# Performance work log

Hardware: AMD Instinct MI355X
Metric: run time of the kernel (lower is better)

The kernel has to match this reference:

```python
import jax, jax.numpy as jnp
import numpy as np
from jax import lax

B, N, NCAM, NLVL = 2, 65536, 5, 3
CIN, MID, OUT, PTSC = 256, 128, 128, 128
H, W = 64, 112
EPS = 1e-3


def setup_inputs() -> dict:
    ks = jax.random.split(jax.random.key(0), 8)
    f32 = jnp.float32
    img_feats = jax.random.normal(ks[0], (NLVL, B * NCAM, CIN, H, W), f32)
    # points roughly in front of the cameras (z ~ 15) so many project in-bounds
    pts_xyz = jax.random.normal(ks[1], (B, N, 3), f32) * 10.0 + jnp.array([0.0, 0.0, 15.0], f32)
    cam_ids = jnp.sort(jax.random.randint(ks[2], (B, N), 0, NCAM), axis=1).astype(jnp.int32)
    pts_feats = jax.random.normal(ks[3], (B * N, PTSC), f32)
    T = jnp.broadcast_to(jnp.eye(4, dtype=f32), (NCAM, 4, 4))
    T = T.at[:, :3, 3].set(jax.random.normal(ks[4], (NCAM, 3), f32) * 0.5)
    fx, fy, cx, cy = 400.0, 400.0, 4.0 * W, 4.0 * H  # full-res intrinsics (feature stride 8)
    K = jnp.broadcast_to(jnp.array([[fx, 0.0, cx], [0.0, fy, cy], [0.0, 0.0, 1.0]], f32), (NCAM, 3, 3))
    conv_w = jax.random.normal(ks[5], (NLVL, MID, CIN, 3, 3), f32) * 0.02
    conv_b = jnp.zeros((NLVL, MID), f32)
    img_w = jax.random.normal(ks[6], (OUT, MID * NLVL), f32) * 0.05
    img_b = jnp.zeros((OUT,), f32)
    img_gamma = jnp.ones((OUT,), f32)
    img_beta = jnp.zeros((OUT,), f32)
    pts_w = jax.random.normal(ks[7], (OUT, PTSC), f32) * 0.05
    pts_b = jnp.zeros((OUT,), f32)
    pts_gamma = jnp.ones((OUT,), f32)
    pts_beta = jnp.zeros((OUT,), f32)
    return dict(img_feats=img_feats, pts_xyz=pts_xyz, pts_feats=pts_feats, T=T, K=K,
                conv_w=conv_w, conv_b=conv_b, img_w=img_w, img_b=img_b,
                img_gamma=img_gamma, img_beta=img_beta, pts_w=pts_w, pts_b=pts_b,
                pts_gamma=pts_gamma, pts_beta=pts_beta, cam_ids=cam_ids)


def _bn(x, gamma, beta):
    # BatchNorm1d in training mode: batch statistics, biased variance, eps=1e-3
    mu = jnp.mean(x, axis=0)
    var = jnp.var(x, axis=0)
    return (x - mu) * lax.rsqrt(var + EPS) * gamma + beta


def _bilinear(feat, bidx, cam, px, py):
    # feat: [B, NCAM, H, W, C]; px/py: [B, N] pixel coords (align_corners=True)
    # grid_sample bilinear with zeros padding: out-of-bounds corners contribute 0
    x0f = jnp.floor(px)
    y0f = jnp.floor(py)
    wx1 = px - x0f
    wy1 = py - y0f

    def corner(xf, yf, wgt):
        valid = (xf >= 0) & (xf <= W - 1) & (yf >= 0) & (yf <= H - 1)
        xi = jnp.clip(xf, 0, W - 1).astype(jnp.int32)
        yi = jnp.clip(yf, 0, H - 1).astype(jnp.int32)
        v = feat[bidx, cam, yi, xi]  # [B, N, C]
        return v * (wgt * valid)[..., None]

    return (corner(x0f, y0f, (1 - wx1) * (1 - wy1))
            + corner(x0f + 1, y0f, wx1 * (1 - wy1))
            + corner(x0f, y0f + 1, (1 - wx1) * wy1)
            + corner(x0f + 1, y0f + 1, wx1 * wy1))


def _forward(img_feats, pts_xyz, pts_feats, T, K, conv_w, conv_b, img_w, img_b,
             img_gamma, img_beta, pts_w, pts_b, pts_gamma, pts_beta, cam_ids):
    # scale intrinsics to the 1/8-resolution feature maps (K[0,0],K[0,2],K[1,1],K[1,2] /= 8)
    k_scale = jnp.array([[0.125, 1.0, 0.125], [1.0, 0.125, 0.125], [1.0, 1.0, 1.0]], jnp.float32)
    Ks = K * k_scale
    ones = jnp.ones(pts_xyz.shape[:2] + (1,), pts_xyz.dtype)
    xyz1 = jnp.concatenate([pts_xyz, ones], axis=-1)      # [B, N, 4]
    Tc = T[cam_ids]                                        # [B, N, 4, 4]
    Kc = Ks[cam_ids]                                       # [B, N, 3, 3]
    pc = jnp.einsum('bnij,bnj->bni', Tc, xyz1)[..., :3]    # camera-frame coords
    pim = jnp.einsum('bnij,bnj->bni', Kc, pc)
    uv = pim[..., :2] / pim[..., 2:3]
    gx = uv[..., 0] / W * 2.0 - 1.0                        # normalized grid coords
    gy = uv[..., 1] / H * 2.0 - 1.0
    px = (gx + 1.0) * 0.5 * (W - 1)                        # align_corners=True mapping
    py = (gy + 1.0) * 0.5 * (H - 1)
    bidx = jnp.broadcast_to(jnp.arange(B)[:, None], cam_ids.shape)
    lvl_feats = []
    for l in range(NLVL):
        f = lax.conv_general_dilated(img_feats[l], conv_w[l], (1, 1), 'SAME',
                                     dimension_numbers=('NCHW', 'OIHW', 'NCHW'))
        f = f + conv_b[l][None, :, None, None]
        f = f.reshape(B, NCAM, MID, H, W).transpose(0, 1, 3, 4, 2)  # [B,NCAM,H,W,C]
        lvl_feats.append(_bilinear(f, bidx, cam_ids, px, py))       # [B,N,MID]
    img_pts = jnp.concatenate(lvl_feats, axis=-1).reshape(B * N, MID * NLVL)
    img_pre = _bn(img_pts @ img_w.T + img_b, img_gamma, img_beta)
    pts_pre = _bn(pts_feats @ pts_w.T + pts_b, pts_gamma, pts_beta)
    return jax.nn.relu(img_pre + pts_pre)


def reference(img_feats, pts_xyz, pts_feats, T, K, conv_w, conv_b, img_w, img_b,
              img_gamma, img_beta, pts_w, pts_b, pts_gamma, pts_beta, cam_ids):
    return _forward(img_feats, pts_xyz, pts_feats, T, K, conv_w, conv_b, img_w, img_b,
                    img_gamma, img_beta, pts_w, pts_b, pts_gamma, pts_beta, cam_ids)
```

## Files before the change

kernel.cpp:

```cpp
#include <hip/hip_runtime.h>
#include <cstdint>

#define LVLPOS 75240
#define GUARD  256
#define NPART  64

using f32x4  = __attribute__((ext_vector_type(4))) float;
using bf16x8 = __attribute__((ext_vector_type(8))) __bf16;

static __device__ __forceinline__ unsigned short f2bf(float f) {
  unsigned int u = __float_as_uint(f);
  u += 0x7fffu + ((u >> 16) & 1u);
  return (unsigned short)(u >> 16);
}
static __device__ __forceinline__ float bflo(uint32_t d) { return __uint_as_float(d << 16); }
static __device__ __forceinline__ float bfhi(uint32_t d) { return __uint_as_float(d & 0xffff0000u); }

#define OFF_WF     ((size_t)0)
#define OFF_BIAS   ((size_t)1769472)
#define OFF_PTSWB  ((size_t)1769984)
#define OFF_STATSP ((size_t)1802752)
#define OFF_FDAT   ((size_t)1933824)
#define OFF_IMGP   ((size_t)21201408)
#define OFF_IRAW   OFF_IMGP
#define OFF_PRAW   (OFF_IMGP + (size_t)33554432)

__global__ __launch_bounds__(256) void k_pre(const float* __restrict__ img,
                                             const float* __restrict__ img_w,
                                             const float* __restrict__ conv_w,
                                             const float* __restrict__ conv_b,
                                             const float* __restrict__ pts_w,
                                             unsigned short* __restrict__ wf,
                                             float* __restrict__ bias,
                                             unsigned short* __restrict__ pts_wb,
                                             unsigned short* __restrict__ imgP,
                                             float* __restrict__ statsP) {
  __shared__ __align__(16) char smem_raw[58368];
  const int t = threadIdx.x;
  if (blockIdx.x < 1920) {
    unsigned short* tile = (unsigned short*)smem_raw;
    const int lvl = blockIdx.x / 640, r = blockIdx.x % 640, n = r >> 6, y = r & 63;
    const float4* src4 = (const float4*)(img + (size_t)(lvl * 10 + n) * 1835008 + (size_t)y * 112);
    for (int v = t; v < 7168; v += 256) {
      int c = v / 28, s = v - c * 28;
      float4 f = src4[(size_t)c * 1792 + s];
      uint2 d;
      d.x = (uint32_t)f2bf(f.x) | ((uint32_t)f2bf(f.y) << 16);
      d.y = (uint32_t)f2bf(f.z) | ((uint32_t)f2bf(f.w) << 16);
      *(uint2*)(tile + c * 114 + s * 4) = d;
    }
    __syncthreads();
    uint32_t* dst = (uint32_t*)(imgP + (size_t)(GUARD + lvl * LVLPOS + (n * 66 + y + 1) * 114) * 256);
    for (int u = t; u < 7296; u += 256) {
      int xp = u >> 6, cp = (u & 63) * 2;
      uint2 val = {0u, 0u};
      if (xp >= 1 && xp <= 112) {
        int x = xp - 1;
        val.x = (uint32_t)tile[(2 * cp) * 114 + x]     | ((uint32_t)tile[(2 * cp + 1) * 114 + x] << 16);
        val.y = (uint32_t)tile[(2 * cp + 2) * 114 + x] | ((uint32_t)tile[(2 * cp + 3) * 114 + x] << 16);
      }
      *(uint2*)(dst + (size_t)xp * 128 + cp) = val;
    }
    return;
  }
  const int b = blockIdx.x - 1920;
  if (b < 432) {
    int z = b >> 1, oh = b & 1;
    int l = z / 72, r = z % 72, tap = r / 8, ckk = r % 8;
    float* iw = (float*)smem_raw;
    float* cw = (float*)smem_raw + 8320;
    for (int v = t; v < 2048; v += 256) {
      int o = v >> 5, seg = v & 31;
      float4 f = *(const float4*)(img_w + (size_t)(oh * 64 + o) * 384 + l * 128 + seg * 4);
      float* d = iw + o * 130 + seg * 4;
      d[0] = f.x; d[1] = f.y; d[2] = f.z; d[3] = f.w;
    }
    for (int v = t; v < 4096; v += 256) {
      int mid = v >> 5, cj = v & 31;
      cw[mid * 33 + cj] = conv_w[(size_t)((l * 128 + mid) * 256 + ckk * 32 + cj) * 9 + tap];
    }
    __syncthreads();
    const int o64 = t & 63, cs = t >> 6, o = oh * 64 + o64;
    float accs[8];
    #pragma unroll
    for (int ci = 0; ci < 8; ++ci) accs[ci] = 0.f;
    for (int mid = 0; mid < 128; ++mid) {
      float a = iw[o64 * 130 + mid];
      #pragma unroll
      for (int ci = 0; ci < 8; ++ci) accs[ci] = fmaf(a, cw[mid * 33 + cs * 8 + ci], accs[ci]);
    }
    #pragma unroll
    for (int ci = 0; ci < 8; ++ci) {
      int c = ckk * 32 + cs * 8 + ci;
      int ck64 = c >> 6, c64 = c & 63;
      int kh = c64 >> 5, kq3 = (c64 >> 3) & 3, el = c64 & 7;
      size_t idx = (size_t)((l * 4 + ck64) * 9 + tap) * 8192
                 + (size_t)(((o >> 4) * 2 + kh) * 512) + ((o & 15) + 16 * kq3) * 8 + el;
      wf[idx] = f2bf(accs[ci]);
    }
  } else if (b < 494) {
    int z = b - 432;
    size_t base; int n16;
    if (z == 60)      { base = 0; n16 = 8192; }
    else if (z == 61) { base = (size_t)(GUARD + 3 * LVLPOS) * 256; n16 = 8192; }
    else {
      int lvl = z / 20, w = z % 20, n = w >> 1, y = (w & 1) ? 65 : 0;
      base = (size_t)(GUARD + lvl * LVLPOS + (n * 66 + y) * 114) * 256; n16 = 3648;
    }
    uint4 zz = {0u, 0u, 0u, 0u};
    uint4* d = (uint4*)(imgP + base);
    for (int v = t; v < n16; v += 256) d[v] = zz;
  } else if (b < 559) {
    int z = b - 494;
    if (z == 0) {
      if (t < 128) {
        float a = 0.f;
        for (int i = 0; i < 384; ++i) a = fmaf(img_w[t * 384 + i], conv_b[i], a);
        bias[t] = a;
      }
    } else {
      int idx = (z - 1) * 256 + t;
      int o = idx >> 7, k = idx & 127;
      int ks = k >> 5, kq = (k >> 3) & 3, el = k & 7;
      int pos = (ks * 8 + (o >> 4)) * 512 + ((o & 15) + 16 * kq) * 8 + el;
      pts_wb[pos] = f2bf(pts_w[idx]);
    }
  } else {
    int z = b - 559;
    ((float4*)statsP)[z * 256 + t] = (float4){0.f, 0.f, 0.f, 0.f};
  }
}

#define APITCH 72
static __device__ __forceinline__ void conv_stage(unsigned short* dst,
                                                  const unsigned short* __restrict__ imgP,
                                                  int s, int m0, int t) {
  int lvl = s / 12, r = s - lvl * 12;
  int ck = r / 3, ky = r - ck * 3;
  const unsigned short* base = imgP
      + (size_t)(GUARD + lvl * LVLPOS + m0 - 1 + (ky - 1) * 114) * 256 + ck * 64;
  for (int v = t; v < 528; v += 256) {
    int p = v >> 3, seg = v & 7;
    *(uint4*)(dst + p * APITCH + seg * 8) = *(const uint4*)(base + (size_t)p * 256 + seg * 8);
  }
}

static __device__ __forceinline__ void conv_compute(const unsigned short* As_,
                                                    const unsigned short* __restrict__ wf,
                                                    int s, int nh, int m, int kq,
                                                    f32x4 (&acc)[4][2]) {
  const unsigned short* W0 = wf + (size_t)(3 * s) * 8192 + (nh * 4) * 512 + (m + 16 * kq) * 8;
  #pragma unroll
  for (int kx = 0; kx < 3; ++kx) {
    const unsigned short* Wp = W0 + kx * 8192;
    bf16x8 bv[2][2];
    #pragma unroll
    for (int nt = 0; nt < 2; ++nt) {
      bv[nt][0] = *(const bf16x8*)(Wp + (nt * 2) * 512);
      bv[nt][1] = *(const bf16x8*)(Wp + (nt * 2 + 1) * 512);
    }
    #pragma unroll
    for (int mt = 0; mt < 4; ++mt) {
      const unsigned short* ap = As_ + (mt * 16 + m + kx) * APITCH + kq * 8;
      bf16x8 a0 = *(const bf16x8*)(ap);
      bf16x8 a1 = *(const bf16x8*)(ap + 32);
      #pragma unroll
      for (int nt = 0; nt < 2; ++nt) {
        acc[mt][nt] = __builtin_amdgcn_mfma_f32_16x16x32_bf16(a0, bv[nt][0], acc[mt][nt], 0, 0, 0);
        acc[mt][nt] = __builtin_amdgcn_mfma_f32_16x16x32_bf16(a1, bv[nt][1], acc[mt][nt], 0, 0, 0);
      }
    }
  }
}

__global__ __launch_bounds__(256, 4) void k_conv(const unsigned short* __restrict__ imgP,
                                                 const unsigned short* __restrict__ wf,
                                                 const float* __restrict__ bias,
                                                 unsigned short* __restrict__ fdat) {
  __shared__ unsigned short As[2][66 * APITCH];
  const int t = threadIdx.x, lane = t & 63, wave = t >> 6;
  const int nh = wave;
  const int m = lane & 15, kq = lane >> 4;
  const int m0 = blockIdx.x * 64;

  f32x4 acc[4][2];
  #pragma unroll
  for (int i = 0; i < 4; ++i)
    #pragma unroll
    for (int j = 0; j < 2; ++j) acc[i][j] = (f32x4){0.f, 0.f, 0.f, 0.f};

  conv_stage(As[0], imgP, 0, m0, t);
  #pragma unroll 1
  for (int s = 0; s < 36; s += 2) {
    __syncthreads();
    if (s + 1 < 36) conv_stage(As[1], imgP, s + 1, m0, t);
    conv_compute(As[0], wf, s, nh, m, kq, acc);
    __syncthreads();
    if (s + 2 < 36) conv_stage(As[0], imgP, s + 2, m0, t);
    conv_compute(As[1], wf, s + 1, nh, m, kq, acc);
  }
  __syncthreads();

  unsigned short* Ep = &As[0][0];
  #pragma unroll
  for (int nt = 0; nt < 2; ++nt) {
    int oc = nh * 32 + nt * 16 + m;
    float bb = bias[oc];
    #pragma unroll
    for (int mt = 0; mt < 4; ++mt)
      #pragma unroll
      for (int rr = 0; rr < 4; ++rr)
        Ep[(mt * 16 + kq * 4 + rr) * 128 + oc] = f2bf(acc[mt][nt][rr] + bb);
  }
  __syncthreads();
  unsigned short* dst = fdat + (size_t)m0 * 128;
  for (int v = t; v < 1024; v += 256)
    *(uint4*)(dst + v * 8) = *(const uint4*)(Ep + v * 8);
}

__global__ __launch_bounds__(256) void k_gp(const float* __restrict__ pts_xyz,
                                            const int* __restrict__ cam_ids,
                                            const float* __restrict__ Tm,
                                            const float* __restrict__ Km,
                                            const unsigned short* __restrict__ fdat,
                                            const float* __restrict__ pts_feats,
                                            const unsigned short* __restrict__ pts_wb,
                                            unsigned short* __restrict__ img_raw,
                                            unsigned short* __restrict__ pts_raw,
                                            float* __restrict__ statsP) {
  __shared__ __align__(16) char smem[19456];
  const int t = threadIdx.x, lane = t & 63, wave = t >> 6;

  if (blockIdx.x < 8192) {
    float* sb = (float*)smem;
    float* qb = sb + 128;
    if (t < 128) { sb[t] = 0.f; sb[128 + t] = 0.f; }
    __syncthreads();
    const int p0 = blockIdx.x * 16 + wave * 4;
    const uint32_t* fq = (const uint32_t*)fdat;
    float s0 = 0.f, q0 = 0.f, s1 = 0.f, q1 = 0.f;
    #pragma unroll 2
    for (int j = 0; j < 4; ++j) {
      const int p = p0 + j;
      const int b = p >> 16;
      const int cam = cam_ids[p];
      const float X = pts_xyz[(size_t)p * 3], Y = pts_xyz[(size_t)p * 3 + 1], Z = pts_xyz[(size_t)p * 3 + 2];
      const float* Tc = Tm + cam * 16;
      float pcx = Tc[0] * X + Tc[1] * Y + Tc[2]  * Z + Tc[3];
      float pcy = Tc[4] * X + Tc[5] * Y + Tc[6]  * Z + Tc[7];
      float pcz = Tc[8] * X + Tc[9] * Y + Tc[10] * Z + Tc[11];
      const float* Kc = Km + cam * 9;
      float pimx = Kc[0] * 0.125f * pcx + Kc[1] * pcy          + Kc[2] * 0.125f * pcz;
      float pimy = Kc[3] * pcx          + Kc[4] * 0.125f * pcy + Kc[5] * 0.125f * pcz;
      float pimz = Kc[6] * pcx          + Kc[7] * pcy          + Kc[8] * pcz;
      float u = pimx / pimz, vv = pimy / pimz;
      float px = (u / 112.f) * 111.f;
      float py = (vv / 64.f) * 63.f;
      float x0 = floorf(px), y0 = floorf(py);
      float wx = px - x0, wy = py - y0;
      float cxf[4] = {x0, x0 + 1.f, x0, x0 + 1.f};
      float cyf[4] = {y0, y0, y0 + 1.f, y0 + 1.f};
      float cwt[4] = {(1.f - wx) * (1.f - wy), wx * (1.f - wy), (1.f - wx) * wy, wx * wy};
      const int nimg = b * 5 + cam;
      float wv[4]; int idx[4]; bool any = false;
      #pragma unroll
      for (int c4 = 0; c4 < 4; ++c4) {
        float xf = cxf[c4], yf = cyf[c4];
        bool valid = (xf >= 0.f) && (xf <= 111.f) && (yf >= 0.f) && (yf <= 63.f);
        float w = cwt[c4] * (valid ? 1.f : 0.f);
        int xi = (int)fminf(fmaxf(xf, 0.f), 111.f);
        int yi = (int)fminf(fmaxf(yf, 0.f), 63.f);
        wv[c4] = w;
        idx[c4] = (nimg * 66 + yi + 1) * 114 + xi + 1;
        any = any || (w != 0.f);
      }
      float a0 = 0.f, a1 = 0.f;
      if (any) {
        #pragma unroll
        for (int c4 = 0; c4 < 4; ++c4) {
          uint32_t d = fq[(size_t)idx[c4] * 64 + lane];
          a0 = fmaf(wv[c4], bflo(d), a0);
          a1 = fmaf(wv[c4], bfhi(d), a1);
        }
      }
      s0 += a0; q0 += a0 * a0; s1 += a1; q1 += a1 * a1;
      ((uint32_t*)img_raw)[(size_t)p * 64 + lane] =
          (uint32_t)f2bf(a0) | ((uint32_t)f2bf(a1) << 16);
    }
    atomicAdd(&sb[lane * 2], s0);
    atomicAdd(&sb[lane * 2 + 1], s1);
    atomicAdd(&qb[lane * 2], q0);
    atomicAdd(&qb[lane * 2 + 1], q1);
    __syncthreads();
    if (t < 128) {
      float* sp = statsP + (size_t)(blockIdx.x & (NPART - 1)) * 512;
      atomicAdd(sp + t, sb[t]);
      atomicAdd(sp + 128 + t, qb[t]);
    }
  } else {
    const int pb = blockIdx.x - 8192;
    const size_t r0 = (size_t)pb * 64;
    unsigned short* As2 = (unsigned short*)smem;
    const int mh = wave & 1, nh = wave >> 1;
    const int m = lane & 15, kq = lane >> 4;
    for (int v = t; v < 2048; v += 256) {
      int mm = v >> 5, seg = v & 31;
      float4 f = *(const float4*)(pts_feats + (r0 + mm) * 128 + seg * 4);
      uint2 d;
      d.x = (uint32_t)f2bf(f.x) | ((uint32_t)f2bf(f.y) << 16);
      d.y = (uint32_t)f2bf(f.z) | ((uint32_t)f2bf(f.w) << 16);
      *(uint2*)(As2 + mm * 136 + seg * 4) = d;
    }
    __syncthreads();
    f32x4 acc[2][4];
    #pragma unroll
    for (int i = 0; i < 2; ++i)
      #pragma unroll
      for (int jj = 0; jj < 4; ++jj) acc[i][jj] = (f32x4){0.f, 0.f, 0.f, 0.f};
    #pragma unroll
    for (int ks = 0; ks < 4; ++ks) {
      bf16x8 af0 = *(const bf16x8*)(As2 + (mh * 32 + 0 * 16 + m) * 136 + ks * 32 + kq * 8);
      bf16x8 af1 = *(const bf16x8*)(As2 + (mh * 32 + 1 * 16 + m) * 136 + ks * 32 + kq * 8);
      #pragma unroll
      for (int nt = 0; nt < 4; ++nt) {
        bf16x8 bv = *(const bf16x8*)(pts_wb + (size_t)((ks * 8 + nh * 4 + nt) * 512) + lane * 8);
        acc[0][nt] = __builtin_amdgcn_mfma_f32_16x16x32_bf16(af0, bv, acc[0][nt], 0, 0, 0);
        acc[1][nt] = __builtin_amdgcn_mfma_f32_16x16x32_bf16(af1, bv, acc[1][nt], 0, 0, 0);
      }
    }
    __syncthreads();
    #pragma unroll
    for (int mt = 0; mt < 2; ++mt)
      #pragma unroll
      for (int nt = 0; nt < 4; ++nt)
        #pragma unroll
        for (int rr = 0; rr < 4; ++rr)
          As2[(mh * 32 + mt * 16 + kq * 4 + rr) * 128 + nh * 64 + nt * 16 + m] = f2bf(acc[mt][nt][rr]);
    __syncthreads();
    unsigned short* dst = pts_raw + r0 * 128;
    for (int v = t; v < 1024; v += 256)
      *(uint4*)(dst + v * 8) = *(const uint4*)(As2 + v * 8);
    float* ps = (float*)(smem + 17408);
    float* pq = (float*)(smem + 18432);
    {
      int col = t & 127, rh = t >> 7;
      float s = 0.f, q = 0.f;
      for (int i = 0; i < 32; ++i) {
        float v = __uint_as_float((uint32_t)As2[(rh * 32 + i) * 128 + col] << 16);
        s += v; q += v * v;
      }
      ps[rh * 128 + col] = s;
      pq[rh * 128 + col] = q;
    }
    __syncthreads();
    if (t < 128) {
      float* sp = statsP + (size_t)(blockIdx.x & (NPART - 1)) * 512;
      atomicAdd(sp + 256 + t, ps[t] + ps[128 + t]);
      atomicAdd(sp + 384 + t, pq[t] + pq[128 + t]);
    }
  }
}

__global__ __launch_bounds__(256) void k_final(const unsigned short* __restrict__ img_raw,
                                               const unsigned short* __restrict__ pts_raw,
                                               const float* __restrict__ statsP,
                                               const float* __restrict__ img_gamma,
                                               const float* __restrict__ img_beta,
                                               const float* __restrict__ pts_gamma,
                                               const float* __restrict__ pts_beta,
                                               float* __restrict__ out) {
  __shared__ float sA[128], sB[128], sC[128];
  const int t = threadIdx.x;
  if (t < 128) {
    float si = 0.f, qi = 0.f, sp = 0.f, qp = 0.f;
    for (int k = 0; k < NPART; ++k) {
      const float* st = statsP + (size_t)k * 512;
      si += st[t]; qi += st[128 + t]; sp += st[256 + t]; qp += st[384 + t];
    }
    const float Nr = 131072.f;
    float mu_i = si / Nr;
    float var_i = qi / Nr - mu_i * mu_i;
    float a_i = img_gamma[t] * rsqrtf(var_i + 1e-3f);
    float mu_p = sp / Nr;
    float var_p = qp / Nr - mu_p * mu_p;
    float a_p = pts_gamma[t] * rsqrtf(var_p + 1e-3f);
    sA[t] = a_i; sB[t] = a_p;
    sC[t] = img_beta[t] + pts_beta[t] - a_i * mu_i - a_p * mu_p;
  }
  __syncthreads();
  const uint32_t* ir = (const uint32_t*)img_raw;
  const uint32_t* pr = (const uint32_t*)pts_raw;
  size_t g0 = (size_t)blockIdx.x * 2048;
  #pragma unroll
  for (int i = 0; i < 4; ++i) {
    size_t g = g0 + (size_t)i * 512 + t * 2;
    uint2 di = *(const uint2*)(ir + g);
    uint2 dp = *(const uint2*)(pr + g);
    int c = (int)(g & 63) * 2;
    float4 o;
    o.x = fmaxf(0.f, sA[c]     * bflo(di.x) + sB[c]     * bflo(dp.x) + sC[c]);
    o.y = fmaxf(0.f, sA[c + 1] * bfhi(di.x) + sB[c + 1] * bfhi(dp.x) + sC[c + 1]);
    o.z = fmaxf(0.f, sA[c + 2] * bflo(di.y) + sB[c + 2] * bflo(dp.y) + sC[c + 2]);
    o.w = fmaxf(0.f, sA[c + 3] * bfhi(di.y) + sB[c + 3] * bfhi(dp.y) + sC[c + 3]);
    *(float4*)(out + g * 2) = o;
  }
}

extern "C" void kernel_launch(void* const* d_in, const int* in_sizes, int n_in,
                              void* d_out, int out_size, void* d_ws, size_t ws_size,
                              hipStream_t stream) {
  const float* img_feats = (const float*)d_in[0];
  const float* pts_xyz   = (const float*)d_in[1];
  const float* pts_feats = (const float*)d_in[2];
  const float* Tm        = (const float*)d_in[3];
  const float* Km        = (const float*)d_in[4];
  const float* conv_w    = (const float*)d_in[5];
  const float* conv_b    = (const float*)d_in[6];
  const float* img_w     = (const float*)d_in[7];
  const float* img_gamma = (const float*)d_in[9];
  const float* img_beta  = (const float*)d_in[10];
  const float* pts_w     = (const float*)d_in[11];
  const float* pts_gamma = (const float*)d_in[13];
  const float* pts_beta  = (const float*)d_in[14];
  const int*   cam_ids   = (const int*)d_in[15];

  char* wsb = (char*)d_ws;
  unsigned short* wf      = (unsigned short*)(wsb + OFF_WF);
  float*          bias    = (float*)(wsb + OFF_BIAS);
  unsigned short* pts_wb  = (unsigned short*)(wsb + OFF_PTSWB);
  float*          statsP  = (float*)(wsb + OFF_STATSP);
  unsigned short* fdat    = (unsigned short*)(wsb + OFF_FDAT);
  unsigned short* imgP    = (unsigned short*)(wsb + OFF_IMGP);
  unsigned short* img_raw = (unsigned short*)(wsb + OFF_IRAW);
  unsigned short* pts_raw = (unsigned short*)(wsb + OFF_PRAW);

  k_pre<<<dim3(2511), dim3(256), 0, stream>>>(img_feats, img_w, conv_w, conv_b, pts_w,
                                              wf, bias, pts_wb, imgP, statsP);
  k_conv<<<dim3(1176), dim3(256), 0, stream>>>(imgP, wf, bias, fdat);
  k_gp<<<dim3(10240), dim3(256), 0, stream>>>(pts_xyz, cam_ids, Tm, Km, fdat,
                                              pts_feats, pts_wb, img_raw, pts_raw, statsP);
  k_final<<<dim3(4096), dim3(256), 0, stream>>>(img_raw, pts_raw, statsP,
                                                img_gamma, img_beta, pts_gamma, pts_beta,
                                                (float*)d_out);
}
```

Measured before the change: 658.0 us.

## Enlarge conv tile to 128 rows per block and hoist BN stats reduction into one kernel

The conv GEMM block grows from 64 to 128 output pixels, with four waves arranged 2x2 over rows and channels, so each weight fragment is reused across more rows and each wave carries a 4x4 accumulator tile. The grid halves to 588 blocks and occupancy drops to two blocks per CU because of the larger register and LDS footprint. Separately, the batch-norm statistics reduction over 64 partitions moves out of every k_final block into a single k_stats kernel that writes the coefficients to workspace, which removes redundant per-block reduction at the cost of one extra launch.

```diff
diff --git a/kernel.cpp b/kernel.cpp
--- a/kernel.cpp
+++ b/kernel.cpp
@@ -24,6 +24,7 @@
 #define OFF_IMGP   ((size_t)21201408)
 #define OFF_IRAW   OFF_IMGP
 #define OFF_PRAW   (OFF_IMGP + (size_t)33554432)
+#define OFF_COEF   (OFF_PRAW + (size_t)33554432)
 
 __global__ __launch_bounds__(256) void k_pre(const float* __restrict__ img,
                                              const float* __restrict__ img_w,
@@ -139,7 +140,7 @@
   int ck = r / 3, ky = r - ck * 3;
   const unsigned short* base = imgP
       + (size_t)(GUARD + lvl * LVLPOS + m0 - 1 + (ky - 1) * 114) * 256 + ck * 64;
-  for (int v = t; v < 528; v += 256) {
+  for (int v = t; v < 1040; v += 256) {
     int p = v >> 3, seg = v & 7;
     *(uint4*)(dst + p * APITCH + seg * 8) = *(const uint4*)(base + (size_t)p * 256 + seg * 8);
   }
@@ -147,25 +148,25 @@
 
 static __device__ __forceinline__ void conv_compute(const unsigned short* As_,
                                                     const unsigned short* __restrict__ wf,
-                                                    int s, int nh, int m, int kq,
-                                                    f32x4 (&acc)[4][2]) {
-  const unsigned short* W0 = wf + (size_t)(3 * s) * 8192 + (nh * 4) * 512 + (m + 16 * kq) * 8;
+                                                    int s, int mh, int nh, int m, int kq,
+                                                    f32x4 (&acc)[4][4]) {
+  const unsigned short* W0 = wf + (size_t)(3 * s) * 8192 + (nh * 8) * 512 + (m + 16 * kq) * 8;
   #pragma unroll
   for (int kx = 0; kx < 3; ++kx) {
     const unsigned short* Wp = W0 + kx * 8192;
-    bf16x8 bv[2][2];
-    #pragma unroll
-    for (int nt = 0; nt < 2; ++nt) {
+    bf16x8 bv[4][2];
+    #pragma unroll
+    for (int nt = 0; nt < 4; ++nt) {
       bv[nt][0] = *(const bf16x8*)(Wp + (nt * 2) * 512);
       bv[nt][1] = *(const bf16x8*)(Wp + (nt * 2 + 1) * 512);
     }
     #pragma unroll
     for (int mt = 0; mt < 4; ++mt) {
-      const unsigned short* ap = As_ + (mt * 16 + m + kx) * APITCH + kq * 8;
+      const unsigned short* ap = As_ + (mh * 64 + mt * 16 + m + kx) * APITCH + kq * 8;
       bf16x8 a0 = *(const bf16x8*)(ap);
       bf16x8 a1 = *(const bf16x8*)(ap + 32);
       #pragma unroll
-      for (int nt = 0; nt < 2; ++nt) {
+      for (int nt = 0; nt < 4; ++nt) {
         acc[mt][nt] = __builtin_amdgcn_mfma_f32_16x16x32_bf16(a0, bv[nt][0], acc[mt][nt], 0, 0, 0);
         acc[mt][nt] = __builtin_amdgcn_mfma_f32_16x16x32_bf16(a1, bv[nt][1], acc[mt][nt], 0, 0, 0);
       }
@@ -173,48 +174,48 @@
   }
 }
 
-__global__ __launch_bounds__(256, 4) void k_conv(const unsigned short* __restrict__ imgP,
+__global__ __launch_bounds__(256, 2) void k_conv(const unsigned short* __restrict__ imgP,
                                                  const unsigned short* __restrict__ wf,
                                                  const float* __restrict__ bias,
                                                  unsigned short* __restrict__ fdat) {
-  __shared__ unsigned short As[2][66 * APITCH];
+  __shared__ unsigned short As[2][130 * APITCH];
   const int t = threadIdx.x, lane = t & 63, wave = t >> 6;
-  const int nh = wave;
+  const int mh = wave & 1, nh = wave >> 1;
   const int m = lane & 15, kq = lane >> 4;
-  const int m0 = blockIdx.x * 64;
-
-  f32x4 acc[4][2];
+  const int m0 = blockIdx.x * 128;
+
+  f32x4 acc[4][4];
   #pragma unroll
   for (int i = 0; i < 4; ++i)
     #pragma unroll
-    for (int j = 0; j < 2; ++j) acc[i][j] = (f32x4){0.f, 0.f, 0.f, 0.f};
+    for (int j = 0; j < 4; ++j) acc[i][j] = (f32x4){0.f, 0.f, 0.f, 0.f};
 
   conv_stage(As[0], imgP, 0, m0, t);
   #pragma unroll 1
   for (int s = 0; s < 36; s += 2) {
     __syncthreads();
     if (s + 1 < 36) conv_stage(As[1], imgP, s + 1, m0, t);
-    conv_compute(As[0], wf, s, nh, m, kq, acc);
+    conv_compute(As[0], wf, s, mh, nh, m, kq, acc);
     __syncthreads();
     if (s + 2 < 36) conv_stage(As[0], imgP, s + 2, m0, t);
-    conv_compute(As[1], wf, s + 1, nh, m, kq, acc);
+    conv_compute(As[1], wf, s + 1, mh, nh, m, kq, acc);
   }
   __syncthreads();
 
   unsigned short* Ep = &As[0][0];
   #pragma unroll
-  for (int nt = 0; nt < 2; ++nt) {
-    int oc = nh * 32 + nt * 16 + m;
+  for (int nt = 0; nt < 4; ++nt) {
+    int oc = nh * 64 + nt * 16 + m;
     float bb = bias[oc];
     #pragma unroll
     for (int mt = 0; mt < 4; ++mt)
       #pragma unroll
       for (int rr = 0; rr < 4; ++rr)
-        Ep[(mt * 16 + kq * 4 + rr) * 128 + oc] = f2bf(acc[mt][nt][rr] + bb);
+        Ep[(mh * 64 + mt * 16 + kq * 4 + rr) * 128 + oc] = f2bf(acc[mt][nt][rr] + bb);
   }
   __syncthreads();
   unsigned short* dst = fdat + (size_t)m0 * 128;
-  for (int v = t; v < 1024; v += 256)
+  for (int v = t; v < 2048; v += 256)
     *(uint4*)(dst + v * 8) = *(const uint4*)(Ep + v * 8);
 }
 
@@ -361,22 +362,23 @@
   }
 }
 
-__global__ __launch_bounds__(256) void k_final(const unsigned short* __restrict__ img_raw,
-                                               const unsigned short* __restrict__ pts_raw,
-                                               const float* __restrict__ statsP,
+__global__ __launch_bounds__(256) void k_stats(const float* __restrict__ statsP,
                                                const float* __restrict__ img_gamma,
                                                const float* __restrict__ img_beta,
                                                const float* __restrict__ pts_gamma,
                                                const float* __restrict__ pts_beta,
-                                               float* __restrict__ out) {
-  __shared__ float sA[128], sB[128], sC[128];
+                                               float* __restrict__ coef) {
+  __shared__ float red[512];
   const int t = threadIdx.x;
+  float s0 = 0.f, s1 = 0.f;
+  for (int k = 0; k < NPART; ++k) {
+    const float* st = statsP + (size_t)k * 512;
+    s0 += st[t]; s1 += st[t + 256];
+  }
+  red[t] = s0; red[t + 256] = s1;
+  __syncthreads();
   if (t < 128) {
-    float si = 0.f, qi = 0.f, sp = 0.f, qp = 0.f;
-    for (int k = 0; k < NPART; ++k) {
-      const float* st = statsP + (size_t)k * 512;
-      si += st[t]; qi += st[128 + t]; sp += st[256 + t]; qp += st[384 + t];
-    }
+    float si = red[t], qi = red[128 + t], sp = red[256 + t], qp = red[384 + t];
     const float Nr = 131072.f;
     float mu_i = si / Nr;
     float var_i = qi / Nr - mu_i * mu_i;
@@ -384,9 +386,19 @@
     float mu_p = sp / Nr;
     float var_p = qp / Nr - mu_p * mu_p;
     float a_p = pts_gamma[t] * rsqrtf(var_p + 1e-3f);
-    sA[t] = a_i; sB[t] = a_p;
-    sC[t] = img_beta[t] + pts_beta[t] - a_i * mu_i - a_p * mu_p;
-  }
+    coef[t] = a_i;
+    coef[128 + t] = a_p;
+    coef[256 + t] = img_beta[t] + pts_beta[t] - a_i * mu_i - a_p * mu_p;
+  }
+}
+
+__global__ __launch_bounds__(256) void k_final(const unsigned short* __restrict__ img_raw,
+                                               const unsigned short* __restrict__ pts_raw,
+                                               const float* __restrict__ coef,
+                                               float* __restrict__ out) {
+  __shared__ float sA[128], sB[128], sC[128];
+  const int t = threadIdx.x;
+  if (t < 128) { sA[t] = coef[t]; sB[t] = coef[128 + t]; sC[t] = coef[256 + t]; }
   __syncthreads();
   const uint32_t* ir = (const uint32_t*)img_raw;
   const uint32_t* pr = (const uint32_t*)pts_raw;
@@ -433,13 +445,14 @@
   unsigned short* imgP    = (unsigned short*)(wsb + OFF_IMGP);
   unsigned short* img_raw = (unsigned short*)(wsb + OFF_IRAW);
   unsigned short* pts_raw = (unsigned short*)(wsb + OFF_PRAW);
+  float*          coef    = (float*)(wsb + OFF_COEF);
 
   k_pre<<<dim3(2511), dim3(256), 0, stream>>>(img_feats, img_w, conv_w, conv_b, pts_w,
                                               wf, bias, pts_wb, imgP, statsP);
-  k_conv<<<dim3(1176), dim3(256), 0, stream>>>(imgP, wf, bias, fdat);
+  k_conv<<<dim3(588), dim3(256), 0, stream>>>(imgP, wf, bias, fdat);
   k_gp<<<dim3(10240), dim3(256), 0, stream>>>(pts_xyz, cam_ids, Tm, Km, fdat,
                                               pts_feats, pts_wb, img_raw, pts_raw, statsP);
-  k_final<<<dim3(4096), dim3(256), 0, stream>>>(img_raw, pts_raw, statsP,
-                                                img_gamma, img_beta, pts_gamma, pts_beta,
-                                                (float*)d_out);
-}
+  k_stats<<<dim3(1), dim3(256), 0, stream>>>(statsP, img_gamma, img_beta,
+                                             pts_gamma, pts_beta, coef);
+  k_final<<<dim3(4096), dim3(256), 0, stream>>>(img_raw, pts_raw, coef, (float*)d_out);
+}
```

Result: slower. 680.4 us (+3.4%).
